# Optimization experiments

Hardware: AMD Instinct MI355X
Metric: run time of the kernel (lower is better)

## Reference

```python
import jax, jax.numpy as jnp
import numpy as np

B, NQ, NK = 16, 512, 1024
CQ, CV = 128, 128
H, D = 8, 64            # nb_heads, attention_size
SCALE = float(np.sqrt(D))


def setup_inputs() -> dict:
    key = jax.random.key(0)
    ks = jax.random.split(key, 10)
    s = 0.02
    return {
        "query": jax.random.normal(ks[0], (B, NQ, CQ), jnp.float32),
        "key": jax.random.normal(ks[1], (B, NK, CV), jnp.float32),
        "c_mask": jax.random.randint(ks[2], (B, NK), 0, 2).astype(jnp.float32),
        # torch Linear params, stored as [in, out] so y = x @ W + b
        "Wq": jax.random.normal(ks[3], (CQ, H * D), jnp.float32) * s,
        "bq": jnp.zeros((H * D,), jnp.float32),
        "Wk": jax.random.normal(ks[4], (CV, H * D), jnp.float32) * s,
        "bk": jnp.zeros((H * D,), jnp.float32),
        "Wv": jax.random.normal(ks[5], (CV, H * D), jnp.float32) * s,
        "bv": jnp.zeros((H * D,), jnp.float32),
    }


def reference(query, key, c_mask, Wq, bq, Wk, bk, Wv, bv):
    # projections -> [B, N, H, D]
    q = (query @ Wq + bq).reshape(B, NQ, H, D)
    k = (key @ Wk + bk).reshape(B, NK, H, D)
    v = (key @ Wv + bv).reshape(B, NK, H, D)
    # scaled scores [B, H, NQ, NK]
    scores = jnp.einsum('bqhd,bkhd->bhqk', q / SCALE, k)
    # additive mask: c_mask [B, NK] broadcasts over heads and queries
    scores = scores - 100000.0 * (1.0 - c_mask[:, None, None, :])
    attn = jax.nn.softmax(scores, axis=-1)
    # weighted values -> [B, NQ, H, D] -> concat heads
    c = jnp.einsum('bhqk,bkhd->bqhd', attn, v)
    return c.reshape(B, NQ, H * D)
```

## Files before the change

kernel.cpp:

```cpp
#include <hip/hip_runtime.h>
#include <hip/hip_bf16.h>

#define B_  16
#define NQ_ 512
#define NK_ 1024
#define CQ_ 128
#define H_  8
#define D_  64
#define HD_ 512

typedef __attribute__((ext_vector_type(8))) short short8;
typedef __attribute__((ext_vector_type(4))) float floatx4;

__device__ __forceinline__ short f2bf(float f) {
    union { float f; unsigned u; } x; x.f = f;
    unsigned r = (x.u + 0x7fffu + ((x.u >> 16) & 1u)) >> 16;
    return (short)r;
}
__device__ __forceinline__ int f2bf_pk(float a, float b) {
    __hip_bfloat162 h = __float22bfloat162_rn(make_float2(a, b));
    int r; __builtin_memcpy(&r, &h, 4); return r;
}
__device__ __forceinline__ short8 pack8(float4 a, float4 b) {
    union { int4 i; short8 s; } u;
    u.i = make_int4(f2bf_pk(a.x, a.y), f2bf_pk(a.z, a.w),
                    f2bf_pk(b.x, b.y), f2bf_pk(b.z, b.w));
    return u.s;
}
__device__ __forceinline__ int2 packi2(floatx4 a) {
    return make_int2(f2bf_pk(a[0], a[1]), f2bf_pk(a[2], a[3]));
}
__device__ __forceinline__ void async16(const short* g, short* l) {
    __builtin_amdgcn_global_load_lds(
        (const __attribute__((address_space(1))) void*)g,
        (__attribute__((address_space(3))) void*)l, 16, 0, 0);
}

__global__ __launch_bounds__(256) void prep_kernel(
    const float* __restrict__ W0, const float* __restrict__ W1,
    const float* __restrict__ W2, short* __restrict__ T0,
    short* __restrict__ T1, short* __restrict__ T2,
    const float* __restrict__ bq, float* __restrict__ bqs, float qscale,
    const float* __restrict__ cmask, int* __restrict__ idx,
    float* __restrict__ cm2, int* __restrict__ npad)
{
    const int blk = blockIdx.x, t = threadIdx.x;
    if (blk == 48) {
        bqs[t]       = bq[t] * qscale;
        bqs[t + 256] = bq[t + 256] * qscale;
        return;
    }
    if (blk >= 49) {
        __shared__ int wsum[4];
        const int b = blk - 49;
        const int w = t >> 6, lane = t & 63;
        float4 m4 = *(const float4*)(cmask + b * NK_ + t * 4);
        const int m0 = m4.x > 0.5f, m1 = m4.y > 0.5f, m2 = m4.z > 0.5f, m3 = m4.w > 0.5f;
        const int s = m0 + m1 + m2 + m3;
        int v = s;
        #pragma unroll
        for (int off = 1; off < 64; off <<= 1) {
            int u = __shfl_up(v, off);
            if (lane >= off) v += u;
        }
        if (lane == 63) wsum[w] = v;
        __syncthreads();
        int pre = 0;
        #pragma unroll
        for (int i = 0; i < 4; ++i) if (i < w) pre += wsum[i];
        int pos = pre + v - s;
        const int base = b * NK_;
        if (m0) { idx[base + pos] = t * 4 + 0; cm2[base + pos] = 1.0f; ++pos; }
        if (m1) { idx[base + pos] = t * 4 + 1; cm2[base + pos] = 1.0f; ++pos; }
        if (m2) { idx[base + pos] = t * 4 + 2; cm2[base + pos] = 1.0f; ++pos; }
        if (m3) { idx[base + pos] = t * 4 + 3; cm2[base + pos] = 1.0f; ++pos; }
        const int total = wsum[0] + wsum[1] + wsum[2] + wsum[3];
        for (int j = total + t; j < NK_; j += 256) {
            idx[base + j] = 0; cm2[base + j] = 0.0f;
        }
        if (t == 0) npad[b] = (total + 127) & ~127;
        return;
    }
    __shared__ short tsh[32 * 132];
    const int mat = blk >> 4, nb = blk & 15;
    const float* W = mat == 0 ? W0 : (mat == 1 ? W1 : W2);
    short* T = mat == 0 ? T0 : (mat == 1 ? T1 : T2);
    const float s = mat == 0 ? qscale : 1.0f;
    #pragma unroll
    for (int i = 0; i < 4; ++i) {
        const int i2 = i * 256 + t;
        const int k = i2 >> 3, c = (i2 & 7) * 4;
        float4 v = *(const float4*)(W + (size_t)k * HD_ + nb * 32 + c);
        tsh[(c + 0) * 132 + k] = f2bf(v.x * s);
        tsh[(c + 1) * 132 + k] = f2bf(v.y * s);
        tsh[(c + 2) * 132 + k] = f2bf(v.z * s);
        tsh[(c + 3) * 132 + k] = f2bf(v.w * s);
    }
    __syncthreads();
    #pragma unroll
    for (int j = 0; j < 2; ++j) {
        const int i2 = j * 256 + t;
        const int n = i2 >> 4, seg = (i2 & 15) * 8;
        *(short8*)(T + (size_t)(nb * 32 + n) * CQ_ + seg) =
            *(const short8*)&tsh[n * 132 + seg];
    }
}

__global__ __launch_bounds__(256, 2) void kvproj_kernel(
    const float* __restrict__ key_,
    const short* __restrict__ wkt, const short* __restrict__ wvt,
    const float* __restrict__ bk, const float* __restrict__ bv,
    short* __restrict__ ks, short* __restrict__ vt,
    const int* __restrict__ idx, const int* __restrict__ npad)
{
    __shared__ __align__(16) short csh[9216];

    int bx = blockIdx.x;
    const short* Wt; const float* bias; short* out; int transposed;
    if (bx < 128) { Wt = wkt; bias = bk; out = ks; transposed = 0; }
    else { bx -= 128; Wt = wvt; bias = bv; out = vt; transposed = 1; }

    const int mbase = bx * 128;
    const int b  = mbase >> 10;
    const int r0 = mbase & 1023;
    if (r0 >= npad[b]) return;

    const int tid  = threadIdx.x;
    const int w    = tid >> 6, lane = tid & 63;
    const int l15  = lane & 15, quad = lane >> 4;
    const int* ib = idx + b * NK_;

    short8 afr[2][4];
    #pragma unroll
    for (int mt = 0; mt < 2; ++mt) {
        const int krow = ib[r0 + w * 32 + mt * 16 + l15];
        const float* xrow = key_ + (size_t)(b * NK_ + krow) * CQ_;
        #pragma unroll
        for (int kt = 0; kt < 4; ++kt)
            afr[mt][kt] = pack8(*(const float4*)(xrow + kt * 32 + quad * 8),
                                *(const float4*)(xrow + kt * 32 + quad * 8 + 4));
    }

    #pragma unroll
    for (int hh = 0; hh < 4; ++hh) {
        const int h = blockIdx.y * 4 + hh;
        short8 bfr[4][4];
        #pragma unroll
        for (int nt = 0; nt < 4; ++nt) {
            const short8* wrow = (const short8*)(Wt + (size_t)(h * 64 + nt * 16 + l15) * CQ_);
            #pragma unroll
            for (int kt = 0; kt < 4; ++kt) bfr[nt][kt] = wrow[kt * 4 + quad];
        }
        floatx4 acc[2][4];
        #pragma unroll
        for (int mt = 0; mt < 2; ++mt)
            #pragma unroll
            for (int nt = 0; nt < 4; ++nt) {
                floatx4 a = {0.f, 0.f, 0.f, 0.f};
                #pragma unroll
                for (int kt = 0; kt < 4; ++kt)
                    a = __builtin_amdgcn_mfma_f32_16x16x32_bf16(afr[mt][kt], bfr[nt][kt], a, 0, 0, 0);
                acc[mt][nt] = a;
            }
        __syncthreads();
        #pragma unroll
        for (int mt = 0; mt < 2; ++mt)
            #pragma unroll
            for (int nt = 0; nt < 4; ++nt) {
                const float bvv = bias[h * 64 + nt * 16 + l15];
                #pragma unroll
                for (int i = 0; i < 4; ++i) {
                    const short s = f2bf(acc[mt][nt][i] + bvv);
                    const int m = w * 32 + mt * 16 + quad * 4 + i;
                    const int n = nt * 16 + l15;
                    if (!transposed) csh[m * 72 + n]  = s;
                    else             csh[n * 136 + m] = s;
                }
            }
        __syncthreads();

        const size_t bh = (size_t)(b * H_ + h);
        if (!transposed) {
            short* dst = out + (bh * NK_ + r0) * D_;
            #pragma unroll
            for (int it = 0; it < 4; ++it) {
                const int i2 = it * 256 + tid;
                const int row = i2 >> 3, c8 = (i2 & 7) * 8;
                *(short8*)(dst + i2 * 8) = *(const short8*)&csh[row * 72 + c8];
            }
        } else {
            short* dst = out + bh * D_ * NK_ + r0;
            #pragma unroll
            for (int it = 0; it < 4; ++it) {
                const int i2 = it * 256 + tid;
                const int row = i2 >> 4, c8 = (i2 & 15) * 8;
                *(short8*)(dst + (size_t)row * NK_ + c8) = *(const short8*)&csh[row * 136 + c8];
            }
        }
    }
}

__global__ __launch_bounds__(256, 2) void attn_kernel(
    const float* __restrict__ query, const short* __restrict__ ks,
    const short* __restrict__ vt, const float* __restrict__ cm2,
    const short* __restrict__ wqt, const float* __restrict__ bqs,
    const int* __restrict__ npad, float* __restrict__ out)
{
    __shared__ __align__(16) short kbuf[2][64 * 64];
    __shared__ __align__(16) short vbuf[2][64 * 64];
    __shared__ __align__(16) short psh[128 * 64];

    const int tid = threadIdx.x;
    const int w = tid >> 6, lane = tid & 63;
    const int l15 = lane & 15, quad = lane >> 4;

    const int bx   = blockIdx.x;
    const int bh_i = bx & 127;
    const int qq   = bx >> 7;
    const int h    = bh_i & 7;
    const int b    = bh_i >> 3;

    const size_t bh = (size_t)bh_i;
    const short* kb_ = ks + bh * NK_ * D_;
    const short* vb  = vt + bh * D_ * NK_;
    const float* mk  = cm2 + (size_t)b * NK_;
    const int nc = npad[b] >> 6;

    short8 qa[2][2];
    {
        short8 waf[4][4];
        #pragma unroll
        for (int dt = 0; dt < 4; ++dt)
            #pragma unroll
            for (int kt = 0; kt < 4; ++kt)
                waf[dt][kt] = *(const short8*)(wqt + (size_t)(h * 64 + dt * 16 + l15) * CQ_ + kt * 32 + quad * 8);
        const int qr0 = qq * 128 + w * 32;
        #pragma unroll
        for (int g = 0; g < 2; ++g) {
            const float* qrow = query + ((size_t)b * NQ_ + qr0 + g * 16 + l15) * CQ_;
            short8 bqf[4];
            #pragma unroll
            for (int kt = 0; kt < 4; ++kt)
                bqf[kt] = pack8(*(const float4*)(qrow + kt * 32 + quad * 8),
                                *(const float4*)(qrow + kt * 32 + quad * 8 + 4));
            const int prow = w * 32 + g * 16 + l15;
            #pragma unroll
            for (int dt = 0; dt < 4; ++dt) {
                float4 bi = *(const float4*)(bqs + h * 64 + dt * 16 + quad * 4);
                floatx4 a = {bi.x, bi.y, bi.z, bi.w};
                #pragma unroll
                for (int kt = 0; kt < 4; ++kt)
                    a = __builtin_amdgcn_mfma_f32_16x16x32_bf16(waf[dt][kt], bqf[kt], a, 0, 0, 0);
                const int c16 = (dt * 2 + (quad >> 1)) ^ (prow & 7);
                *(int2*)&psh[prow * 64 + c16 * 8 + (quad & 1) * 4] = packi2(a);
            }
            qa[g][0] = *(const short8*)&psh[prow * 64 + ((quad    ) ^ (prow & 7)) * 8];
            qa[g][1] = *(const short8*)&psh[prow * 64 + ((4 + quad) ^ (prow & 7)) * 8];
        }
    }

    const int srow8 = lane >> 3, sc = lane & 7;
    auto stage = [&](int kb0, short* kdst, short* vdst) {
        #pragma unroll
        for (int j = 0; j < 2; ++j) {
            const int row = w * 16 + j * 8 + srow8;
            const int cs = sc ^ (row & 7);
            async16(kb_ + (size_t)(kb0 + row) * D_ + cs * 8, &kdst[(w * 16 + j * 8) * 64]);
            async16(vb + (size_t)row * NK_ + kb0 + cs * 8, &vdst[(w * 16 + j * 8) * 64]);
        }
    };

    float l_lane[2] = {0.f, 0.f};
    floatx4 o_acc[2][4];
    #pragma unroll
    for (int g = 0; g < 2; ++g)
        #pragma unroll
        for (int dt = 0; dt < 4; ++dt) o_acc[g][dt] = (floatx4){0.f, 0.f, 0.f, 0.f};

    stage(0, kbuf[0], vbuf[0]);
    __syncthreads();

    for (int t = 0; t < nc; ++t) {
        const int cur = t & 1;
        if (t + 1 < nc) stage((t + 1) * 64, kbuf[cur ^ 1], vbuf[cur ^ 1]);
        const short* kb  = kbuf[cur];
        const short* vbl = vbuf[cur];
        const int kbase = t * 64;

        short8 ka[4][2];
        #pragma unroll
        for (int nt = 0; nt < 4; ++nt) {
            const int row = nt * 16 + l15;
            ka[nt][0] = *(const short8*)&kb[row * 64 + ((quad    ) ^ (row & 7)) * 8];
            ka[nt][1] = *(const short8*)&kb[row * 64 + ((4 + quad) ^ (row & 7)) * 8];
        }
        short8 vf[2][4];
        #pragma unroll
        for (int dt = 0; dt < 4; ++dt) {
            const int row = dt * 16 + l15;
            vf[0][dt] = *(const short8*)&vbl[row * 64 + ((quad    ) ^ (row & 7)) * 8];
            vf[1][dt] = *(const short8*)&vbl[row * 64 + ((4 + quad) ^ (row & 7)) * 8];
        }
        float4 m4[4];
        #pragma unroll
        for (int nt = 0; nt < 4; ++nt)
            m4[nt] = *(const float4*)(mk + kbase + nt * 16 + quad * 4);

        #pragma unroll
        for (int g = 0; g < 2; ++g) {
            floatx4 st[4];
            #pragma unroll
            for (int nt = 0; nt < 4; ++nt) {
                floatx4 a = {0.f, 0.f, 0.f, 0.f};
                a = __builtin_amdgcn_mfma_f32_16x16x32_bf16(ka[nt][1], qa[g][1], a, 0, 0, 0);
                a = __builtin_amdgcn_mfma_f32_16x16x32_bf16(ka[nt][0], qa[g][0], a, 0, 0, 0);
                st[nt] = a;
            }
            const int prow = w * 32 + g * 16 + l15;
            float psum = 0.f;
            #pragma unroll
            for (int nt = 0; nt < 4; ++nt) {
                float p0 = m4[nt].x * __builtin_amdgcn_exp2f(st[nt][0]);
                float p1 = m4[nt].y * __builtin_amdgcn_exp2f(st[nt][1]);
                float p2 = m4[nt].z * __builtin_amdgcn_exp2f(st[nt][2]);
                float p3 = m4[nt].w * __builtin_amdgcn_exp2f(st[nt][3]);
                psum += (p0 + p1) + (p2 + p3);
                int2 pk = make_int2(f2bf_pk(p0, p1), f2bf_pk(p2, p3));
                const int c16 = (2 * nt + (quad >> 1)) ^ (prow & 7);
                *(int2*)&psh[prow * 64 + c16 * 8 + (quad & 1) * 4] = pk;
            }
            l_lane[g] += psum;
            #pragma unroll
            for (int kt = 0; kt < 2; ++kt) {
                short8 pa = *(const short8*)&psh[prow * 64 + ((kt * 4 + quad) ^ (prow & 7)) * 8];
                #pragma unroll
                for (int dt = 0; dt < 4; ++dt)
                    o_acc[g][dt] = __builtin_amdgcn_mfma_f32_16x16x32_bf16(vf[kt][dt], pa, o_acc[g][dt], 0, 0, 0);
            }
        }
        __syncthreads();
    }

    #pragma unroll
    for (int g = 0; g < 2; ++g) {
        float ls = l_lane[g];
        ls += __shfl_xor(ls, 16);
        ls += __shfl_xor(ls, 32);
        const float linv = 1.0f / ls;
        const int qr = qq * 128 + w * 32 + g * 16 + l15;
        float* orow = out + ((size_t)b * NQ_ + qr) * HD_ + h * D_;
        #pragma unroll
        for (int dt = 0; dt < 4; ++dt) {
            float4 v = make_float4(o_acc[g][dt][0] * linv, o_acc[g][dt][1] * linv,
                                   o_acc[g][dt][2] * linv, o_acc[g][dt][3] * linv);
            *(float4*)(orow + dt * 16 + quad * 4) = v;
        }
    }
}

extern "C" void kernel_launch(void* const* d_in, const int* in_sizes, int n_in,
                              void* d_out, int out_size, void* d_ws, size_t ws_size,
                              hipStream_t stream) {
    const float* query = (const float*)d_in[0];
    const float* key   = (const float*)d_in[1];
    const float* cmask = (const float*)d_in[2];
    const float* Wq    = (const float*)d_in[3];
    const float* bq    = (const float*)d_in[4];
    const float* Wk    = (const float*)d_in[5];
    const float* bk    = (const float*)d_in[6];
    const float* Wv    = (const float*)d_in[7];
    const float* bv    = (const float*)d_in[8];
    float* out = (float*)d_out;

    char* ws = (char*)d_ws;
    short* ks  = (short*)(ws);
    short* vt  = (short*)(ws + (size_t)(16u << 20));
    char*  w32 = ws + (size_t)(32u << 20);
    short* wqt = (short*)(w32);
    short* wkt = (short*)(w32 + 131072);
    short* wvt = (short*)(w32 + 131072 * 2);
    float* bqs = (float*)(w32 + 131072 * 3);
    int*   idx = (int*)(w32 + 131072 * 3 + 4096);
    float* cm2 = (float*)(w32 + 131072 * 3 + 4096 + 65536);
    int*  npad = (int*)(w32 + 131072 * 3 + 4096 + 131072);

    const float qscale = 0.125f * 1.44269504f;
    prep_kernel<<<dim3(65), dim3(256), 0, stream>>>(
        Wq, Wk, Wv, wqt, wkt, wvt, bq, bqs, qscale, cmask, idx, cm2, npad);

    kvproj_kernel<<<dim3(256, 2), dim3(256), 0, stream>>>(
        key, wkt, wvt, bk, bv, ks, vt, idx, npad);

    attn_kernel<<<dim3(512), dim3(256), 0, stream>>>(
        query, ks, vt, cm2, wqt, bqs, npad, out);
}
```

Before: 136.7 us.

## Fuse prep, KV projection and attention into one persistent kernel with grid barriers

Merges the three separate launches (weight prep and mask compaction, K/V projection, attention) into a single 512-block kernel. The phases are separated by a software grid barrier built on a global atomic counter, which is reset with a memset before each launch. The aim is to remove the launch gaps and tail effects between kernels. The barrier is correct only if all 512 blocks are resident at the same time, which needs 2 blocks per CU on 256 CUs. The spin loop has a timeout break, and if it fires the phases could read incomplete data.

```diff
diff --git a/kernel.cpp b/kernel.cpp
--- a/kernel.cpp
+++ b/kernel.cpp
@@ -36,324 +36,336 @@
         (__attribute__((address_space(3))) void*)l, 16, 0, 0);
 }
 
-__global__ __launch_bounds__(256) void prep_kernel(
-    const float* __restrict__ W0, const float* __restrict__ W1,
-    const float* __restrict__ W2, short* __restrict__ T0,
-    short* __restrict__ T1, short* __restrict__ T2,
-    const float* __restrict__ bq, float* __restrict__ bqs, float qscale,
-    const float* __restrict__ cmask, int* __restrict__ idx,
-    float* __restrict__ cm2, int* __restrict__ npad)
-{
-    const int blk = blockIdx.x, t = threadIdx.x;
-    if (blk == 48) {
-        bqs[t]       = bq[t] * qscale;
-        bqs[t + 256] = bq[t + 256] * qscale;
-        return;
-    }
-    if (blk >= 49) {
-        __shared__ int wsum[4];
-        const int b = blk - 49;
-        const int w = t >> 6, lane = t & 63;
-        float4 m4 = *(const float4*)(cmask + b * NK_ + t * 4);
-        const int m0 = m4.x > 0.5f, m1 = m4.y > 0.5f, m2 = m4.z > 0.5f, m3 = m4.w > 0.5f;
-        const int s = m0 + m1 + m2 + m3;
-        int v = s;
-        #pragma unroll
-        for (int off = 1; off < 64; off <<= 1) {
-            int u = __shfl_up(v, off);
-            if (lane >= off) v += u;
-        }
-        if (lane == 63) wsum[w] = v;
-        __syncthreads();
-        int pre = 0;
-        #pragma unroll
-        for (int i = 0; i < 4; ++i) if (i < w) pre += wsum[i];
-        int pos = pre + v - s;
-        const int base = b * NK_;
-        if (m0) { idx[base + pos] = t * 4 + 0; cm2[base + pos] = 1.0f; ++pos; }
-        if (m1) { idx[base + pos] = t * 4 + 1; cm2[base + pos] = 1.0f; ++pos; }
-        if (m2) { idx[base + pos] = t * 4 + 2; cm2[base + pos] = 1.0f; ++pos; }
-        if (m3) { idx[base + pos] = t * 4 + 3; cm2[base + pos] = 1.0f; ++pos; }
-        const int total = wsum[0] + wsum[1] + wsum[2] + wsum[3];
-        for (int j = total + t; j < NK_; j += 256) {
-            idx[base + j] = 0; cm2[base + j] = 0.0f;
-        }
-        if (t == 0) npad[b] = (total + 127) & ~127;
-        return;
-    }
-    __shared__ short tsh[32 * 132];
-    const int mat = blk >> 4, nb = blk & 15;
-    const float* W = mat == 0 ? W0 : (mat == 1 ? W1 : W2);
-    short* T = mat == 0 ? T0 : (mat == 1 ? T1 : T2);
-    const float s = mat == 0 ? qscale : 1.0f;
-    #pragma unroll
-    for (int i = 0; i < 4; ++i) {
-        const int i2 = i * 256 + t;
-        const int k = i2 >> 3, c = (i2 & 7) * 4;
-        float4 v = *(const float4*)(W + (size_t)k * HD_ + nb * 32 + c);
-        tsh[(c + 0) * 132 + k] = f2bf(v.x * s);
-        tsh[(c + 1) * 132 + k] = f2bf(v.y * s);
-        tsh[(c + 2) * 132 + k] = f2bf(v.z * s);
-        tsh[(c + 3) * 132 + k] = f2bf(v.w * s);
+__device__ __forceinline__ void grid_sync(unsigned* bar, unsigned target) {
+    __syncthreads();
+    if (threadIdx.x == 0) {
+        __threadfence();
+        atomicAdd(bar, 1u);
+        long long t0 = clock64();
+        while (__hip_atomic_load(bar, __ATOMIC_RELAXED, __HIP_MEMORY_SCOPE_AGENT) < target) {
+            __builtin_amdgcn_s_sleep(4);
+            if (clock64() - t0 > (1ll << 31)) break;
+        }
+        __threadfence();
     }
     __syncthreads();
-    #pragma unroll
-    for (int j = 0; j < 2; ++j) {
-        const int i2 = j * 256 + t;
-        const int n = i2 >> 4, seg = (i2 & 15) * 8;
-        *(short8*)(T + (size_t)(nb * 32 + n) * CQ_ + seg) =
-            *(const short8*)&tsh[n * 132 + seg];
+}
+
+__global__ __launch_bounds__(256, 2) void fused_kernel(
+    const float* __restrict__ query, const float* __restrict__ key_,
+    const float* __restrict__ cmask,
+    const float* __restrict__ Wq, const float* __restrict__ bq,
+    const float* __restrict__ Wk, const float* __restrict__ bk,
+    const float* __restrict__ Wv, const float* __restrict__ bv,
+    short* __restrict__ wqt, short* __restrict__ wkt, short* __restrict__ wvt,
+    float* __restrict__ bqs, int* __restrict__ idx, float* __restrict__ cm2,
+    int* __restrict__ npad, short* __restrict__ ks, short* __restrict__ vt,
+    unsigned* __restrict__ bar, float* __restrict__ out)
+{
+    __shared__ __align__(16) char smem[49152];
+    const int tid = threadIdx.x;
+    const float qscale = 0.125f * 1.44269504f;
+
+    {
+        const int blk = blockIdx.x;
+        if (blk == 48) {
+            bqs[tid]       = bq[tid] * qscale;
+            bqs[tid + 256] = bq[tid + 256] * qscale;
+        } else if (blk >= 49 && blk < 65) {
+            int* wsum = (int*)smem;
+            const int t = tid;
+            const int b = blk - 49;
+            const int w = t >> 6, lane = t & 63;
+            float4 m4 = *(const float4*)(cmask + b * NK_ + t * 4);
+            const int m0 = m4.x > 0.5f, m1 = m4.y > 0.5f, m2 = m4.z > 0.5f, m3 = m4.w > 0.5f;
+            const int s = m0 + m1 + m2 + m3;
+            int v = s;
+            #pragma unroll
+            for (int off = 1; off < 64; off <<= 1) {
+                int u = __shfl_up(v, off);
+                if (lane >= off) v += u;
+            }
+            if (lane == 63) wsum[w] = v;
+            __syncthreads();
+            int pre = 0;
+            #pragma unroll
+            for (int i = 0; i < 4; ++i) if (i < w) pre += wsum[i];
+            int pos = pre + v - s;
+            const int base = b * NK_;
+            if (m0) { idx[base + pos] = t * 4 + 0; cm2[base + pos] = 1.0f; ++pos; }
+            if (m1) { idx[base + pos] = t * 4 + 1; cm2[base + pos] = 1.0f; ++pos; }
+            if (m2) { idx[base + pos] = t * 4 + 2; cm2[base + pos] = 1.0f; ++pos; }
+            if (m3) { idx[base + pos] = t * 4 + 3; cm2[base + pos] = 1.0f; ++pos; }
+            const int total = wsum[0] + wsum[1] + wsum[2] + wsum[3];
+            for (int j = total + t; j < NK_; j += 256) {
+                idx[base + j] = 0; cm2[base + j] = 0.0f;
+            }
+            if (t == 0) npad[b] = (total + 127) & ~127;
+        } else if (blk < 48) {
+            short* tsh = (short*)smem;
+            const int mat = blk >> 4, nb = blk & 15;
+            const float* W = mat == 0 ? Wq : (mat == 1 ? Wk : Wv);
+            short* T = mat == 0 ? wqt : (mat == 1 ? wkt : wvt);
+            const float s = mat == 0 ? qscale : 1.0f;
+            #pragma unroll
+            for (int i = 0; i < 4; ++i) {
+                const int i2 = i * 256 + tid;
+                const int k = i2 >> 3, c = (i2 & 7) * 4;
+                float4 v = *(const float4*)(W + (size_t)k * HD_ + nb * 32 + c);
+                tsh[(c + 0) * 132 + k] = f2bf(v.x * s);
+                tsh[(c + 1) * 132 + k] = f2bf(v.y * s);
+                tsh[(c + 2) * 132 + k] = f2bf(v.z * s);
+                tsh[(c + 3) * 132 + k] = f2bf(v.w * s);
+            }
+            __syncthreads();
+            #pragma unroll
+            for (int j = 0; j < 2; ++j) {
+                const int i2 = j * 256 + tid;
+                const int n = i2 >> 4, seg = (i2 & 15) * 8;
+                *(short8*)(T + (size_t)(nb * 32 + n) * CQ_ + seg) =
+                    *(const short8*)&tsh[n * 132 + seg];
+            }
+        }
     }
-}
-
-__global__ __launch_bounds__(256, 2) void kvproj_kernel(
-    const float* __restrict__ key_,
-    const short* __restrict__ wkt, const short* __restrict__ wvt,
-    const float* __restrict__ bk, const float* __restrict__ bv,
-    short* __restrict__ ks, short* __restrict__ vt,
-    const int* __restrict__ idx, const int* __restrict__ npad)
-{
-    __shared__ __align__(16) short csh[9216];
-
-    int bx = blockIdx.x;
-    const short* Wt; const float* bias; short* out; int transposed;
-    if (bx < 128) { Wt = wkt; bias = bk; out = ks; transposed = 0; }
-    else { bx -= 128; Wt = wvt; bias = bv; out = vt; transposed = 1; }
-
-    const int mbase = bx * 128;
-    const int b  = mbase >> 10;
-    const int r0 = mbase & 1023;
-    if (r0 >= npad[b]) return;
-
-    const int tid  = threadIdx.x;
-    const int w    = tid >> 6, lane = tid & 63;
-    const int l15  = lane & 15, quad = lane >> 4;
-    const int* ib = idx + b * NK_;
-
-    short8 afr[2][4];
-    #pragma unroll
-    for (int mt = 0; mt < 2; ++mt) {
-        const int krow = ib[r0 + w * 32 + mt * 16 + l15];
-        const float* xrow = key_ + (size_t)(b * NK_ + krow) * CQ_;
+    grid_sync(bar, gridDim.x);
+
+    {
+        int bx = blockIdx.x & 255;
+        const int by = blockIdx.x >> 8;
+        const short* Wt; const float* bias; short* op; int transposed;
+        if (bx < 128) { Wt = wkt; bias = bk; op = ks; transposed = 0; }
+        else { bx -= 128; Wt = wvt; bias = bv; op = vt; transposed = 1; }
+
+        const int mbase = bx * 128;
+        const int b  = mbase >> 10;
+        const int r0 = mbase & 1023;
+        if (r0 < npad[b]) {
+            short* csh = (short*)smem;
+            const int w    = tid >> 6, lane = tid & 63;
+            const int l15  = lane & 15, quad = lane >> 4;
+            const int* ib = idx + b * NK_;
+
+            short8 afr[2][4];
+            #pragma unroll
+            for (int mt = 0; mt < 2; ++mt) {
+                const int krow = ib[r0 + w * 32 + mt * 16 + l15];
+                const float* xrow = key_ + (size_t)(b * NK_ + krow) * CQ_;
+                #pragma unroll
+                for (int kt = 0; kt < 4; ++kt)
+                    afr[mt][kt] = pack8(*(const float4*)(xrow + kt * 32 + quad * 8),
+                                        *(const float4*)(xrow + kt * 32 + quad * 8 + 4));
+            }
+
+            #pragma unroll
+            for (int hh = 0; hh < 4; ++hh) {
+                const int h = by * 4 + hh;
+                short8 bfr[4][4];
+                #pragma unroll
+                for (int nt = 0; nt < 4; ++nt) {
+                    const short8* wrow = (const short8*)(Wt + (size_t)(h * 64 + nt * 16 + l15) * CQ_);
+                    #pragma unroll
+                    for (int kt = 0; kt < 4; ++kt) bfr[nt][kt] = wrow[kt * 4 + quad];
+                }
+                floatx4 acc[2][4];
+                #pragma unroll
+                for (int mt = 0; mt < 2; ++mt)
+                    #pragma unroll
+                    for (int nt = 0; nt < 4; ++nt) {
+                        floatx4 a = {0.f, 0.f, 0.f, 0.f};
+                        #pragma unroll
+                        for (int kt = 0; kt < 4; ++kt)
+                            a = __builtin_amdgcn_mfma_f32_16x16x32_bf16(afr[mt][kt], bfr[nt][kt], a, 0, 0, 0);
+                        acc[mt][nt] = a;
+                    }
+                __syncthreads();
+                #pragma unroll
+                for (int mt = 0; mt < 2; ++mt)
+                    #pragma unroll
+                    for (int nt = 0; nt < 4; ++nt) {
+                        const float bvv = bias[h * 64 + nt * 16 + l15];
+                        #pragma unroll
+                        for (int i = 0; i < 4; ++i) {
+                            const short sv = f2bf(acc[mt][nt][i] + bvv);
+                            const int m = w * 32 + mt * 16 + quad * 4 + i;
+                            const int n = nt * 16 + l15;
+                            if (!transposed) csh[m * 72 + n]  = sv;
+                            else             csh[n * 136 + m] = sv;
+                        }
+                    }
+                __syncthreads();
+
+                const size_t bh = (size_t)(b * H_ + h);
+                if (!transposed) {
+                    short* dst = op + (bh * NK_ + r0) * D_;
+                    #pragma unroll
+                    for (int it = 0; it < 4; ++it) {
+                        const int i2 = it * 256 + tid;
+                        const int row = i2 >> 3, c8 = (i2 & 7) * 8;
+                        *(short8*)(dst + i2 * 8) = *(const short8*)&csh[row * 72 + c8];
+                    }
+                } else {
+                    short* dst = op + bh * D_ * NK_ + r0;
+                    #pragma unroll
+                    for (int it = 0; it < 4; ++it) {
+                        const int i2 = it * 256 + tid;
+                        const int row = i2 >> 4, c8 = (i2 & 15) * 8;
+                        *(short8*)(dst + (size_t)row * NK_ + c8) = *(const short8*)&csh[row * 136 + c8];
+                    }
+                }
+            }
+        }
+    }
+    grid_sync(bar, 2u * gridDim.x);
+
+    {
+        short* const klds = (short*)smem;
+        short* const vlds = (short*)smem + 8192;
+        short* const psh  = (short*)smem + 16384;
+
+        const int w = tid >> 6, lane = tid & 63;
+        const int l15 = lane & 15, quad = lane >> 4;
+
+        const int bx   = blockIdx.x;
+        const int bh_i = bx & 127;
+        const int qq   = bx >> 7;
+        const int h    = bh_i & 7;
+        const int b    = bh_i >> 3;
+
+        const size_t bh = (size_t)bh_i;
+        const short* kb_ = ks + bh * NK_ * D_;
+        const short* vb  = vt + bh * D_ * NK_;
+        const float* mk  = cm2 + (size_t)b * NK_;
+        const int nc = npad[b] >> 6;
+
+        short8 qa[2][2];
+        {
+            short8 waf[4][4];
+            #pragma unroll
+            for (int dt = 0; dt < 4; ++dt)
+                #pragma unroll
+                for (int kt = 0; kt < 4; ++kt)
+                    waf[dt][kt] = *(const short8*)(wqt + (size_t)(h * 64 + dt * 16 + l15) * CQ_ + kt * 32 + quad * 8);
+            const int qr0 = qq * 128 + w * 32;
+            #pragma unroll
+            for (int g = 0; g < 2; ++g) {
+                const float* qrow = query + ((size_t)b * NQ_ + qr0 + g * 16 + l15) * CQ_;
+                short8 bqf[4];
+                #pragma unroll
+                for (int kt = 0; kt < 4; ++kt)
+                    bqf[kt] = pack8(*(const float4*)(qrow + kt * 32 + quad * 8),
+                                    *(const float4*)(qrow + kt * 32 + quad * 8 + 4));
+                const int prow = w * 32 + g * 16 + l15;
+                #pragma unroll
+                for (int dt = 0; dt < 4; ++dt) {
+                    float4 bi = *(const float4*)(bqs + h * 64 + dt * 16 + quad * 4);
+                    floatx4 a = {bi.x, bi.y, bi.z, bi.w};
+                    #pragma unroll
+                    for (int kt = 0; kt < 4; ++kt)
+                        a = __builtin_amdgcn_mfma_f32_16x16x32_bf16(waf[dt][kt], bqf[kt], a, 0, 0, 0);
+                    const int c16 = (dt * 2 + (quad >> 1)) ^ (prow & 7);
+                    *(int2*)&psh[prow * 64 + c16 * 8 + (quad & 1) * 4] = packi2(a);
+                }
+                qa[g][0] = *(const short8*)&psh[prow * 64 + ((quad    ) ^ (prow & 7)) * 8];
+                qa[g][1] = *(const short8*)&psh[prow * 64 + ((4 + quad) ^ (prow & 7)) * 8];
+            }
+        }
+
+        const int srow8 = lane >> 3, sc = lane & 7;
+        auto stage = [&](int kc, short* kdst, short* vdst) {
+            #pragma unroll
+            for (int j = 0; j < 2; ++j) {
+                const int row = w * 16 + j * 8 + srow8;
+                const int cs = sc ^ (row & 7);
+                async16(kb_ + (size_t)(kc + row) * D_ + cs * 8, &kdst[(w * 16 + j * 8) * 64]);
+                async16(vb + (size_t)row * NK_ + kc + cs * 8, &vdst[(w * 16 + j * 8) * 64]);
+            }
+        };
+
+        float l_lane[2] = {0.f, 0.f};
+        floatx4 o_acc[2][4];
         #pragma unroll
-        for (int kt = 0; kt < 4; ++kt)
-            afr[mt][kt] = pack8(*(const float4*)(xrow + kt * 32 + quad * 8),
-                                *(const float4*)(xrow + kt * 32 + quad * 8 + 4));
-    }
-
-    #pragma unroll
-    for (int hh = 0; hh < 4; ++hh) {
-        const int h = blockIdx.y * 4 + hh;
-        short8 bfr[4][4];
-        #pragma unroll
-        for (int nt = 0; nt < 4; ++nt) {
-            const short8* wrow = (const short8*)(Wt + (size_t)(h * 64 + nt * 16 + l15) * CQ_);
-            #pragma unroll
-            for (int kt = 0; kt < 4; ++kt) bfr[nt][kt] = wrow[kt * 4 + quad];
-        }
-        floatx4 acc[2][4];
-        #pragma unroll
-        for (int mt = 0; mt < 2; ++mt)
+        for (int g = 0; g < 2; ++g)
+            #pragma unroll
+            for (int dt = 0; dt < 4; ++dt) o_acc[g][dt] = (floatx4){0.f, 0.f, 0.f, 0.f};
+
+        stage(0, klds, vlds);
+        __syncthreads();
+
+        for (int t = 0; t < nc; ++t) {
+            const int cur = t & 1;
+            if (t + 1 < nc) stage((t + 1) * 64, klds + (cur ^ 1) * 4096, vlds + (cur ^ 1) * 4096);
+            const short* kb  = klds + cur * 4096;
+            const short* vbl = vlds + cur * 4096;
+            const int kbase = t * 64;
+
+            short8 ka[4][2];
             #pragma unroll
             for (int nt = 0; nt < 4; ++nt) {
-                floatx4 a = {0.f, 0.f, 0.f, 0.f};
-                #pragma unroll
-                for (int kt = 0; kt < 4; ++kt)
-                    a = __builtin_amdgcn_mfma_f32_16x16x32_bf16(afr[mt][kt], bfr[nt][kt], a, 0, 0, 0);
-                acc[mt][nt] = a;
-            }
-        __syncthreads();
-        #pragma unroll
-        for (int mt = 0; mt < 2; ++mt)
-            #pragma unroll
-            for (int nt = 0; nt < 4; ++nt) {
-                const float bvv = bias[h * 64 + nt * 16 + l15];
-                #pragma unroll
-                for (int i = 0; i < 4; ++i) {
-                    const short s = f2bf(acc[mt][nt][i] + bvv);
-                    const int m = w * 32 + mt * 16 + quad * 4 + i;
-                    const int n = nt * 16 + l15;
-                    if (!transposed) csh[m * 72 + n]  = s;
-                    else             csh[n * 136 + m] = s;
-                }
-            }
-        __syncthreads();
-
-        const size_t bh = (size_t)(b * H_ + h);
-        if (!transposed) {
-            short* dst = out + (bh * NK_ + r0) * D_;
-            #pragma unroll
-            for (int it = 0; it < 4; ++it) {
-                const int i2 = it * 256 + tid;
-                const int row = i2 >> 3, c8 = (i2 & 7) * 8;
-                *(short8*)(dst + i2 * 8) = *(const short8*)&csh[row * 72 + c8];
-            }
-        } else {
-            short* dst = out + bh * D_ * NK_ + r0;
-            #pragma unroll
-            for (int it = 0; it < 4; ++it) {
-                const int i2 = it * 256 + tid;
-                const int row = i2 >> 4, c8 = (i2 & 15) * 8;
-                *(short8*)(dst + (size_t)row * NK_ + c8) = *(const short8*)&csh[row * 136 + c8];
-            }
-        }
-    }
-}
-
-__global__ __launch_bounds__(256, 2) void attn_kernel(
-    const float* __restrict__ query, const short* __restrict__ ks,
-    const short* __restrict__ vt, const float* __restrict__ cm2,
-    const short* __restrict__ wqt, const float* __restrict__ bqs,
-    const int* __restrict__ npad, float* __restrict__ out)
-{
-    __shared__ __align__(16) short kbuf[2][64 * 64];
-    __shared__ __align__(16) short vbuf[2][64 * 64];
-    __shared__ __align__(16) short psh[128 * 64];
-
-    const int tid = threadIdx.x;
-    const int w = tid >> 6, lane = tid & 63;
-    const int l15 = lane & 15, quad = lane >> 4;
-
-    const int bx   = blockIdx.x;
-    const int bh_i = bx & 127;
-    const int qq   = bx >> 7;
-    const int h    = bh_i & 7;
-    const int b    = bh_i >> 3;
-
-    const size_t bh = (size_t)bh_i;
-    const short* kb_ = ks + bh * NK_ * D_;
-    const short* vb  = vt + bh * D_ * NK_;
-    const float* mk  = cm2 + (size_t)b * NK_;
-    const int nc = npad[b] >> 6;
-
-    short8 qa[2][2];
-    {
-        short8 waf[4][4];
-        #pragma unroll
-        for (int dt = 0; dt < 4; ++dt)
-            #pragma unroll
-            for (int kt = 0; kt < 4; ++kt)
-                waf[dt][kt] = *(const short8*)(wqt + (size_t)(h * 64 + dt * 16 + l15) * CQ_ + kt * 32 + quad * 8);
-        const int qr0 = qq * 128 + w * 32;
+                const int row = nt * 16 + l15;
+                ka[nt][0] = *(const short8*)&kb[row * 64 + ((quad    ) ^ (row & 7)) * 8];
+                ka[nt][1] = *(const short8*)&kb[row * 64 + ((4 + quad) ^ (row & 7)) * 8];
+            }
+            short8 vf[2][4];
+            #pragma unroll
+            for (int dt = 0; dt < 4; ++dt) {
+                const int row = dt * 16 + l15;
+                vf[0][dt] = *(const short8*)&vbl[row * 64 + ((quad    ) ^ (row & 7)) * 8];
+                vf[1][dt] = *(const short8*)&vbl[row * 64 + ((4 + quad) ^ (row & 7)) * 8];
+            }
+            float4 m4[4];
+            #pragma unroll
+            for (int nt = 0; nt < 4; ++nt)
+                m4[nt] = *(const float4*)(mk + kbase + nt * 16 + quad * 4);
+
+            #pragma unroll
+            for (int g = 0; g < 2; ++g) {
+                floatx4 st[4];
+                #pragma unroll
+                for (int nt = 0; nt < 4; ++nt) {
+                    floatx4 a = {0.f, 0.f, 0.f, 0.f};
+                    a = __builtin_amdgcn_mfma_f32_16x16x32_bf16(ka[nt][1], qa[g][1], a, 0, 0, 0);
+                    a = __builtin_amdgcn_mfma_f32_16x16x32_bf16(ka[nt][0], qa[g][0], a, 0, 0, 0);
+                    st[nt] = a;
+                }
+                const int prow = w * 32 + g * 16 + l15;
+                float psum = 0.f;
+                #pragma unroll
+                for (int nt = 0; nt < 4; ++nt) {
+                    float p0 = m4[nt].x * __builtin_amdgcn_exp2f(st[nt][0]);
+                    float p1 = m4[nt].y * __builtin_amdgcn_exp2f(st[nt][1]);
+                    float p2 = m4[nt].z * __builtin_amdgcn_exp2f(st[nt][2]);
+                    float p3 = m4[nt].w * __builtin_amdgcn_exp2f(st[nt][3]);
+                    psum += (p0 + p1) + (p2 + p3);
+                    int2 pk = make_int2(f2bf_pk(p0, p1), f2bf_pk(p2, p3));
+                    const int c16 = (2 * nt + (quad >> 1)) ^ (prow & 7);
+                    *(int2*)&psh[prow * 64 + c16 * 8 + (quad & 1) * 4] = pk;
+                }
+                l_lane[g] += psum;
+                #pragma unroll
+                for (int kt = 0; kt < 2; ++kt) {
+                    short8 pa = *(const short8*)&psh[prow * 64 + ((kt * 4 + quad) ^ (prow & 7)) * 8];
+                    #pragma unroll
+                    for (int dt = 0; dt < 4; ++dt)
+                        o_acc[g][dt] = __builtin_amdgcn_mfma_f32_16x16x32_bf16(vf[kt][dt], pa, o_acc[g][dt], 0, 0, 0);
+                }
+            }
+            __syncthreads();
+        }
+
         #pragma unroll
         for (int g = 0; g < 2; ++g) {
-            const float* qrow = query + ((size_t)b * NQ_ + qr0 + g * 16 + l15) * CQ_;
-            short8 bqf[4];
-            #pragma unroll
-            for (int kt = 0; kt < 4; ++kt)
-                bqf[kt] = pack8(*(const float4*)(qrow + kt * 32 + quad * 8),
-                                *(const float4*)(qrow + kt * 32 + quad * 8 + 4));
-            const int prow = w * 32 + g * 16 + l15;
+            float ls = l_lane[g];
+            ls += __shfl_xor(ls, 16);
+            ls += __shfl_xor(ls, 32);
+            const float linv = 1.0f / ls;
+            const int qr = qq * 128 + w * 32 + g * 16 + l15;
+            float* orow = out + ((size_t)b * NQ_ + qr) * HD_ + h * D_;
             #pragma unroll
             for (int dt = 0; dt < 4; ++dt) {
-                float4 bi = *(const float4*)(bqs + h * 64 + dt * 16 + quad * 4);
-                floatx4 a = {bi.x, bi.y, bi.z, bi.w};
-                #pragma unroll
-                for (int kt = 0; kt < 4; ++kt)
-                    a = __builtin_amdgcn_mfma_f32_16x16x32_bf16(waf[dt][kt], bqf[kt], a, 0, 0, 0);
-                const int c16 = (dt * 2 + (quad >> 1)) ^ (prow & 7);
-                *(int2*)&psh[prow * 64 + c16 * 8 + (quad & 1) * 4] = packi2(a);
-            }
-            qa[g][0] = *(const short8*)&psh[prow * 64 + ((quad    ) ^ (prow & 7)) * 8];
-            qa[g][1] = *(const short8*)&psh[prow * 64 + ((4 + quad) ^ (prow & 7)) * 8];
-        }
-    }
-
-    const int srow8 = lane >> 3, sc = lane & 7;
-    auto stage = [&](int kb0, short* kdst, short* vdst) {
-        #pragma unroll
-        for (int j = 0; j < 2; ++j) {
-            const int row = w * 16 + j * 8 + srow8;
-            const int cs = sc ^ (row & 7);
-            async16(kb_ + (size_t)(kb0 + row) * D_ + cs * 8, &kdst[(w * 16 + j * 8) * 64]);
-            async16(vb + (size_t)row * NK_ + kb0 + cs * 8, &vdst[(w * 16 + j * 8) * 64]);
-        }
-    };
-
-    float l_lane[2] = {0.f, 0.f};
-    floatx4 o_acc[2][4];
-    #pragma unroll
-    for (int g = 0; g < 2; ++g)
-        #pragma unroll
-        for (int dt = 0; dt < 4; ++dt) o_acc[g][dt] = (floatx4){0.f, 0.f, 0.f, 0.f};
-
-    stage(0, kbuf[0], vbuf[0]);
-    __syncthreads();
-
-    for (int t = 0; t < nc; ++t) {
-        const int cur = t & 1;
-        if (t + 1 < nc) stage((t + 1) * 64, kbuf[cur ^ 1], vbuf[cur ^ 1]);
-        const short* kb  = kbuf[cur];
-        const short* vbl = vbuf[cur];
-        const int kbase = t * 64;
-
-        short8 ka[4][2];
-        #pragma unroll
-        for (int nt = 0; nt < 4; ++nt) {
-            const int row = nt * 16 + l15;
-            ka[nt][0] = *(const short8*)&kb[row * 64 + ((quad    ) ^ (row & 7)) * 8];
-            ka[nt][1] = *(const short8*)&kb[row * 64 + ((4 + quad) ^ (row & 7)) * 8];
-        }
-        short8 vf[2][4];
-        #pragma unroll
-        for (int dt = 0; dt < 4; ++dt) {
-            const int row = dt * 16 + l15;
-            vf[0][dt] = *(const short8*)&vbl[row * 64 + ((quad    ) ^ (row & 7)) * 8];
-            vf[1][dt] = *(const short8*)&vbl[row * 64 + ((4 + quad) ^ (row & 7)) * 8];
-        }
-        float4 m4[4];
-        #pragma unroll
-        for (int nt = 0; nt < 4; ++nt)
-            m4[nt] = *(const float4*)(mk + kbase + nt * 16 + quad * 4);
-
-        #pragma unroll
-        for (int g = 0; g < 2; ++g) {
-            floatx4 st[4];
-            #pragma unroll
-            for (int nt = 0; nt < 4; ++nt) {
-                floatx4 a = {0.f, 0.f, 0.f, 0.f};
-                a = __builtin_amdgcn_mfma_f32_16x16x32_bf16(ka[nt][1], qa[g][1], a, 0, 0, 0);
-                a = __builtin_amdgcn_mfma_f32_16x16x32_bf16(ka[nt][0], qa[g][0], a, 0, 0, 0);
-                st[nt] = a;
-            }
-            const int prow = w * 32 + g * 16 + l15;
-            float psum = 0.f;
-            #pragma unroll
-            for (int nt = 0; nt < 4; ++nt) {
-                float p0 = m4[nt].x * __builtin_amdgcn_exp2f(st[nt][0]);
-                float p1 = m4[nt].y * __builtin_amdgcn_exp2f(st[nt][1]);
-                float p2 = m4[nt].z * __builtin_amdgcn_exp2f(st[nt][2]);
-                float p3 = m4[nt].w * __builtin_amdgcn_exp2f(st[nt][3]);
-                psum += (p0 + p1) + (p2 + p3);
-                int2 pk = make_int2(f2bf_pk(p0, p1), f2bf_pk(p2, p3));
-                const int c16 = (2 * nt + (quad >> 1)) ^ (prow & 7);
-                *(int2*)&psh[prow * 64 + c16 * 8 + (quad & 1) * 4] = pk;
-            }
-            l_lane[g] += psum;
-            #pragma unroll
-            for (int kt = 0; kt < 2; ++kt) {
-                short8 pa = *(const short8*)&psh[prow * 64 + ((kt * 4 + quad) ^ (prow & 7)) * 8];
-                #pragma unroll
-                for (int dt = 0; dt < 4; ++dt)
-                    o_acc[g][dt] = __builtin_amdgcn_mfma_f32_16x16x32_bf16(vf[kt][dt], pa, o_acc[g][dt], 0, 0, 0);
-            }
-        }
-        __syncthreads();
-    }
-
-    #pragma unroll
-    for (int g = 0; g < 2; ++g) {
-        float ls = l_lane[g];
-        ls += __shfl_xor(ls, 16);
-        ls += __shfl_xor(ls, 32);
-        const float linv = 1.0f / ls;
-        const int qr = qq * 128 + w * 32 + g * 16 + l15;
-        float* orow = out + ((size_t)b * NQ_ + qr) * HD_ + h * D_;
-        #pragma unroll
-        for (int dt = 0; dt < 4; ++dt) {
-            float4 v = make_float4(o_acc[g][dt][0] * linv, o_acc[g][dt][1] * linv,
-                                   o_acc[g][dt][2] * linv, o_acc[g][dt][3] * linv);
-            *(float4*)(orow + dt * 16 + quad * 4) = v;
+                float4 v = make_float4(o_acc[g][dt][0] * linv, o_acc[g][dt][1] * linv,
+                                       o_acc[g][dt][2] * linv, o_acc[g][dt][3] * linv);
+                *(float4*)(orow + dt * 16 + quad * 4) = v;
+            }
         }
     }
 }
@@ -383,14 +395,11 @@
     int*   idx = (int*)(w32 + 131072 * 3 + 4096);
     float* cm2 = (float*)(w32 + 131072 * 3 + 4096 + 65536);
     int*  npad = (int*)(w32 + 131072 * 3 + 4096 + 131072);
-
-    const float qscale = 0.125f * 1.44269504f;
-    prep_kernel<<<dim3(65), dim3(256), 0, stream>>>(
-        Wq, Wk, Wv, wqt, wkt, wvt, bq, bqs, qscale, cmask, idx, cm2, npad);
-
-    kvproj_kernel<<<dim3(256, 2), dim3(256), 0, stream>>>(
-        key, wkt, wvt, bk, bv, ks, vt, idx, npad);
-
-    attn_kernel<<<dim3(512), dim3(256), 0, stream>>>(
-        query, ks, vt, cm2, wqt, bqs, npad, out);
-}
+    unsigned* bar = (unsigned*)(ws + (size_t)(40u << 20));
+
+    hipMemsetAsync(bar, 0, 64, stream);
+
+    fused_kernel<<<dim3(512), dim3(256), 0, stream>>>(
+        query, key, cmask, Wq, bq, Wk, bk, Wv, bv,
+        wqt, wkt, wvt, bqs, idx, cm2, npad, ks, vt, bar, out);
+}
```

After: 215.6 us. 57.7% more time.

## Halve per-block work in attention and KV projection to double grid size

Applied to the files above, without the earlier changes.

The attention kernel now processes 64 query rows per block (16 per wave) instead of 128, which doubles the grid to 1024 blocks and shrinks the P staging buffer. The KV projection kernel handles 2 heads per block instead of 4, doubling its grid. Both kernels raise the launch-bounds occupancy hint from 2 to 4 blocks per CU. The aim is better CU fill and latency hiding. The cost is that each K/V tile loaded into shared memory, and each key-row fragment in the projection, is reused across fewer rows, so K/V and key traffic roughly doubles.

```diff
diff --git a/kernel.cpp b/kernel.cpp
--- a/kernel.cpp
+++ b/kernel.cpp
@@ -106,7 +106,7 @@
     }
 }
 
-__global__ __launch_bounds__(256, 2) void kvproj_kernel(
+__global__ __launch_bounds__(256, 4) void kvproj_kernel(
     const float* __restrict__ key_,
     const short* __restrict__ wkt, const short* __restrict__ wvt,
     const float* __restrict__ bk, const float* __restrict__ bv,
@@ -142,8 +142,8 @@
     }
 
     #pragma unroll
-    for (int hh = 0; hh < 4; ++hh) {
-        const int h = blockIdx.y * 4 + hh;
+    for (int hh = 0; hh < 2; ++hh) {
+        const int h = blockIdx.y * 2 + hh;
         short8 bfr[4][4];
         #pragma unroll
         for (int nt = 0; nt < 4; ++nt) {
@@ -200,7 +200,7 @@
     }
 }
 
-__global__ __launch_bounds__(256, 2) void attn_kernel(
+__global__ __launch_bounds__(256, 4) void attn_kernel(
     const float* __restrict__ query, const short* __restrict__ ks,
     const short* __restrict__ vt, const float* __restrict__ cm2,
     const short* __restrict__ wqt, const float* __restrict__ bqs,
@@ -208,7 +208,7 @@
 {
     __shared__ __align__(16) short kbuf[2][64 * 64];
     __shared__ __align__(16) short vbuf[2][64 * 64];
-    __shared__ __align__(16) short psh[128 * 64];
+    __shared__ __align__(16) short psh[64 * 64];
 
     const int tid = threadIdx.x;
     const int w = tid >> 6, lane = tid & 63;
@@ -226,7 +226,9 @@
     const float* mk  = cm2 + (size_t)b * NK_;
     const int nc = npad[b] >> 6;
 
-    short8 qa[2][2];
+    const int prow = w * 16 + l15;
+
+    short8 qa[2];
     {
         short8 waf[4][4];
         #pragma unroll
@@ -234,29 +236,24 @@
             #pragma unroll
             for (int kt = 0; kt < 4; ++kt)
                 waf[dt][kt] = *(const short8*)(wqt + (size_t)(h * 64 + dt * 16 + l15) * CQ_ + kt * 32 + quad * 8);
-        const int qr0 = qq * 128 + w * 32;
-        #pragma unroll
-        for (int g = 0; g < 2; ++g) {
-            const float* qrow = query + ((size_t)b * NQ_ + qr0 + g * 16 + l15) * CQ_;
-            short8 bqf[4];
+        const float* qrow = query + ((size_t)b * NQ_ + qq * 64 + prow) * CQ_;
+        short8 bqf[4];
+        #pragma unroll
+        for (int kt = 0; kt < 4; ++kt)
+            bqf[kt] = pack8(*(const float4*)(qrow + kt * 32 + quad * 8),
+                            *(const float4*)(qrow + kt * 32 + quad * 8 + 4));
+        #pragma unroll
+        for (int dt = 0; dt < 4; ++dt) {
+            float4 bi = *(const float4*)(bqs + h * 64 + dt * 16 + quad * 4);
+            floatx4 a = {bi.x, bi.y, bi.z, bi.w};
             #pragma unroll
             for (int kt = 0; kt < 4; ++kt)
-                bqf[kt] = pack8(*(const float4*)(qrow + kt * 32 + quad * 8),
-                                *(const float4*)(qrow + kt * 32 + quad * 8 + 4));
-            const int prow = w * 32 + g * 16 + l15;
-            #pragma unroll
-            for (int dt = 0; dt < 4; ++dt) {
-                float4 bi = *(const float4*)(bqs + h * 64 + dt * 16 + quad * 4);
-                floatx4 a = {bi.x, bi.y, bi.z, bi.w};
-                #pragma unroll
-                for (int kt = 0; kt < 4; ++kt)
-                    a = __builtin_amdgcn_mfma_f32_16x16x32_bf16(waf[dt][kt], bqf[kt], a, 0, 0, 0);
-                const int c16 = (dt * 2 + (quad >> 1)) ^ (prow & 7);
-                *(int2*)&psh[prow * 64 + c16 * 8 + (quad & 1) * 4] = packi2(a);
-            }
-            qa[g][0] = *(const short8*)&psh[prow * 64 + ((quad    ) ^ (prow & 7)) * 8];
-            qa[g][1] = *(const short8*)&psh[prow * 64 + ((4 + quad) ^ (prow & 7)) * 8];
-        }
+                a = __builtin_amdgcn_mfma_f32_16x16x32_bf16(waf[dt][kt], bqf[kt], a, 0, 0, 0);
+            const int c16 = (dt * 2 + (quad >> 1)) ^ (prow & 7);
+            *(int2*)&psh[prow * 64 + c16 * 8 + (quad & 1) * 4] = packi2(a);
+        }
+        qa[0] = *(const short8*)&psh[prow * 64 + ((quad    ) ^ (prow & 7)) * 8];
+        qa[1] = *(const short8*)&psh[prow * 64 + ((4 + quad) ^ (prow & 7)) * 8];
     }
 
     const int srow8 = lane >> 3, sc = lane & 7;
@@ -270,12 +267,10 @@
         }
     };
 
-    float l_lane[2] = {0.f, 0.f};
-    floatx4 o_acc[2][4];
-    #pragma unroll
-    for (int g = 0; g < 2; ++g)
-        #pragma unroll
-        for (int dt = 0; dt < 4; ++dt) o_acc[g][dt] = (floatx4){0.f, 0.f, 0.f, 0.f};
+    float l_lane = 0.f;
+    floatx4 o_acc[4];
+    #pragma unroll
+    for (int dt = 0; dt < 4; ++dt) o_acc[dt] = (floatx4){0.f, 0.f, 0.f, 0.f};
 
     stage(0, kbuf[0], vbuf[0]);
     __syncthreads();
@@ -306,53 +301,48 @@
         for (int nt = 0; nt < 4; ++nt)
             m4[nt] = *(const float4*)(mk + kbase + nt * 16 + quad * 4);
 
-        #pragma unroll
-        for (int g = 0; g < 2; ++g) {
-            floatx4 st[4];
-            #pragma unroll
-            for (int nt = 0; nt < 4; ++nt) {
-                floatx4 a = {0.f, 0.f, 0.f, 0.f};
-                a = __builtin_amdgcn_mfma_f32_16x16x32_bf16(ka[nt][1], qa[g][1], a, 0, 0, 0);
-                a = __builtin_amdgcn_mfma_f32_16x16x32_bf16(ka[nt][0], qa[g][0], a, 0, 0, 0);
-                st[nt] = a;
-            }
-            const int prow = w * 32 + g * 16 + l15;
-            float psum = 0.f;
-            #pragma unroll
-            for (int nt = 0; nt < 4; ++nt) {
-                float p0 = m4[nt].x * __builtin_amdgcn_exp2f(st[nt][0]);
-                float p1 = m4[nt].y * __builtin_amdgcn_exp2f(st[nt][1]);
-                float p2 = m4[nt].z * __builtin_amdgcn_exp2f(st[nt][2]);
-                float p3 = m4[nt].w * __builtin_amdgcn_exp2f(st[nt][3]);
-                psum += (p0 + p1) + (p2 + p3);
-                int2 pk = make_int2(f2bf_pk(p0, p1), f2bf_pk(p2, p3));
-                const int c16 = (2 * nt + (quad >> 1)) ^ (prow & 7);
-                *(int2*)&psh[prow * 64 + c16 * 8 + (quad & 1) * 4] = pk;
-            }
-            l_lane[g] += psum;
-            #pragma unroll
-            for (int kt = 0; kt < 2; ++kt) {
-                short8 pa = *(const short8*)&psh[prow * 64 + ((kt * 4 + quad) ^ (prow & 7)) * 8];
-                #pragma unroll
-                for (int dt = 0; dt < 4; ++dt)
-                    o_acc[g][dt] = __builtin_amdgcn_mfma_f32_16x16x32_bf16(vf[kt][dt], pa, o_acc[g][dt], 0, 0, 0);
-            }
+        floatx4 st[4];
+        #pragma unroll
+        for (int nt = 0; nt < 4; ++nt) {
+            floatx4 a = {0.f, 0.f, 0.f, 0.f};
+            a = __builtin_amdgcn_mfma_f32_16x16x32_bf16(ka[nt][1], qa[1], a, 0, 0, 0);
+            a = __builtin_amdgcn_mfma_f32_16x16x32_bf16(ka[nt][0], qa[0], a, 0, 0, 0);
+            st[nt] = a;
+        }
+        float psum = 0.f;
+        #pragma unroll
+        for (int nt = 0; nt < 4; ++nt) {
+            float p0 = m4[nt].x * __builtin_amdgcn_exp2f(st[nt][0]);
+            float p1 = m4[nt].y * __builtin_amdgcn_exp2f(st[nt][1]);
+            float p2 = m4[nt].z * __builtin_amdgcn_exp2f(st[nt][2]);
+            float p3 = m4[nt].w * __builtin_amdgcn_exp2f(st[nt][3]);
+            psum += (p0 + p1) + (p2 + p3);
+            int2 pk = make_int2(f2bf_pk(p0, p1), f2bf_pk(p2, p3));
+            const int c16 = (2 * nt + (quad >> 1)) ^ (prow & 7);
+            *(int2*)&psh[prow * 64 + c16 * 8 + (quad & 1) * 4] = pk;
+        }
+        l_lane += psum;
+        #pragma unroll
+        for (int kt = 0; kt < 2; ++kt) {
+            short8 pa = *(const short8*)&psh[prow * 64 + ((kt * 4 + quad) ^ (prow & 7)) * 8];
+            #pragma unroll
+            for (int dt = 0; dt < 4; ++dt)
+                o_acc[dt] = __builtin_amdgcn_mfma_f32_16x16x32_bf16(vf[kt][dt], pa, o_acc[dt], 0, 0, 0);
         }
         __syncthreads();
     }
 
-    #pragma unroll
-    for (int g = 0; g < 2; ++g) {
-        float ls = l_lane[g];
+    {
+        float ls = l_lane;
         ls += __shfl_xor(ls, 16);
         ls += __shfl_xor(ls, 32);
         const float linv = 1.0f / ls;
-        const int qr = qq * 128 + w * 32 + g * 16 + l15;
+        const int qr = qq * 64 + prow;
         float* orow = out + ((size_t)b * NQ_ + qr) * HD_ + h * D_;
         #pragma unroll
         for (int dt = 0; dt < 4; ++dt) {
-            float4 v = make_float4(o_acc[g][dt][0] * linv, o_acc[g][dt][1] * linv,
-                                   o_acc[g][dt][2] * linv, o_acc[g][dt][3] * linv);
+            float4 v = make_float4(o_acc[dt][0] * linv, o_acc[dt][1] * linv,
+                                   o_acc[dt][2] * linv, o_acc[dt][3] * linv);
             *(float4*)(orow + dt * 16 + quad * 4) = v;
         }
     }
@@ -388,9 +378,9 @@
     prep_kernel<<<dim3(65), dim3(256), 0, stream>>>(
         Wq, Wk, Wv, wqt, wkt, wvt, bq, bqs, qscale, cmask, idx, cm2, npad);
 
-    kvproj_kernel<<<dim3(256, 2), dim3(256), 0, stream>>>(
+    kvproj_kernel<<<dim3(256, 4), dim3(256), 0, stream>>>(
         key, wkt, wvt, bk, bv, ks, vt, idx, npad);
 
-    attn_kernel<<<dim3(512), dim3(256), 0, stream>>>(
+    attn_kernel<<<dim3(1024), dim3(256), 0, stream>>>(
         query, ks, vt, cm2, wqt, bqs, npad, out);
 }
```

Measured after the change: 139.7 us. 2.2% more time.
